# Optimization experiments

Hardware: AMD Instinct MI355X
Metric: run time of the kernel (lower is better)

## Reference

```python
import jax, jax.numpy as jnp
import numpy as np

B, S, D = 32, 512, 768
H = 12
HD = D // H
SCALE = HD ** -0.5


def setup_inputs() -> dict:
    key = jax.random.key(0)
    ks = jax.random.split(key, 5)
    return {
        "x": jax.random.normal(ks[0], (B, S, D), dtype=jnp.float32),
        "qkv_w": jax.random.normal(ks[1], (3 * D, D), dtype=jnp.float32) * (D ** -0.5),
        "qkv_b": jax.random.normal(ks[2], (3 * D,), dtype=jnp.float32) * 0.02,
        "proj_w": jax.random.normal(ks[3], (D, D), dtype=jnp.float32) * (D ** -0.5),
        "proj_b": jax.random.normal(ks[4], (D,), dtype=jnp.float32) * 0.02,
    }


def reference(x, qkv_w, qkv_b, proj_w, proj_b) -> jnp.ndarray:
    b, s, d = x.shape
    # fused QKV projection (torch Linear: x @ W.T + b)
    qkv = x @ qkv_w.T + qkv_b                      # [B,S,3D]
    qkv = qkv.reshape(b, s, 3, H, HD)
    qkv = jnp.transpose(qkv, (2, 0, 3, 1, 4))      # [3,B,H,S,HD]
    q, k, v = qkv[0], qkv[1], qkv[2]
    scores = jnp.einsum("bhqd,bhkd->bhqk", q, k) * SCALE  # [B,H,S,S]
    # attn_drop with p=0.0 (eval) -> identity
    attn = jax.nn.softmax(scores, axis=-1)
    out = jnp.einsum("bhqk,bhkd->bhqd", attn, v)   # [B,H,S,HD]
    out = jnp.transpose(out, (0, 2, 1, 3)).reshape(b, s, d)
    out = out @ proj_w.T + proj_b                  # proj_drop p=0.0 -> identity
    return out
```

## Files before the change

### kernel.cpp

```cpp
#include <hip/hip_runtime.h>
#include <hip/hip_bf16.h>

#define B_  32
#define S_  512
#define D_  768
#define H_  12
#define HD_ 64
#define QKV_ELEMS (B_ * H_ * S_ * HD_)

typedef __hip_bfloat16 bf16;
typedef short bf16x8_t __attribute__((ext_vector_type(8)));
typedef float f32x4_t  __attribute__((ext_vector_type(4)));

__device__ __forceinline__ float bf2f(bf16 x) { return __bfloat162float(x); }
__device__ __forceinline__ bf16  f2bf(float x) { return __float2bfloat16(x); }

__device__ __forceinline__ void gl_lds16(const short* g, short* l) {
    __builtin_amdgcn_global_load_lds(
        (const __attribute__((address_space(1))) void*)g,
        (__attribute__((address_space(3))) void*)l, 16, 0, 0);
}

__global__ __launch_bounds__(256) void f2bf_kernel(
    const float* __restrict__ in, unsigned short* __restrict__ out, int n4)
{
    int i = blockIdx.x * 256 + threadIdx.x;
    if (i >= n4) return;
    float4 v = reinterpret_cast<const float4*>(in)[i];
    ushort4 o;
    o.x = __bfloat16_as_ushort(f2bf(v.x));
    o.y = __bfloat16_as_ushort(f2bf(v.y));
    o.z = __bfloat16_as_ushort(f2bf(v.z));
    o.w = __bfloat16_as_ushort(f2bf(v.w));
    reinterpret_cast<ushort4*>(out)[i] = o;
}

#define GEMM_CORE(As, Bs, Aptr, Bptr, m0, n0, K)                               \
    const int t = threadIdx.x;                                                 \
    const int w = t >> 6, lane = t & 63;                                       \
    const int wr = w >> 1, wc = w & 1;                                         \
    const int quad = lane >> 4, l16 = lane & 15;                               \
    f32x4_t acc[4][4] = {};                                                    \
    const int lrow = lane >> 3;                                                \
    const int scol = (((lane & 7) ^ (lrow & 7)) * 8);                          \
    _Pragma("unroll")                                                          \
    for (int j = 0; j < 4; ++j) {                                              \
        int R = j * 32 + w * 8;                                                \
        gl_lds16((Aptr) + (size_t)((m0) + R + lrow) * (K) + scol, &(As)[R * 64]); \
        gl_lds16((Bptr) + (size_t)((n0) + R + lrow) * (K) + scol, &(Bs)[R * 64]); \
    }                                                                          \
    for (int k0 = 0; k0 < (K); k0 += 64) {                                     \
        const int curo = ((k0 >> 6) & 1) * 8192;                               \
        __syncthreads();                                                       \
        if (k0 + 64 < (K)) {                                                   \
            const int nxo = curo ^ 8192;                                       \
            _Pragma("unroll")                                                  \
            for (int j = 0; j < 4; ++j) {                                      \
                int R = j * 32 + w * 8;                                        \
                gl_lds16((Aptr) + (size_t)((m0) + R + lrow) * (K) + k0 + 64 + scol, \
                         &(As)[nxo + R * 64]);                                 \
                gl_lds16((Bptr) + (size_t)((n0) + R + lrow) * (K) + k0 + 64 + scol, \
                         &(Bs)[nxo + R * 64]);                                 \
            }                                                                  \
        }                                                                      \
        _Pragma("unroll")                                                      \
        for (int ks = 0; ks < 64; ks += 32) {                                  \
            bf16x8_t af[4], bf_[4];                                            \
            _Pragma("unroll")                                                  \
            for (int tm = 0; tm < 4; ++tm)                                     \
                af[tm] = *(const bf16x8_t*)&(As)[curo + (wr * 64 + tm * 16 + l16) * 64 \
                        + ((((ks >> 3) + quad) ^ (l16 & 7)) * 8)];             \
            _Pragma("unroll")                                                  \
            for (int tn = 0; tn < 4; ++tn)                                     \
                bf_[tn] = *(const bf16x8_t*)&(Bs)[curo + (wc * 64 + tn * 16 + l16) * 64 \
                        + ((((ks >> 3) + quad) ^ (l16 & 7)) * 8)];             \
            _Pragma("unroll")                                                  \
            for (int tm = 0; tm < 4; ++tm)                                     \
                _Pragma("unroll")                                              \
                for (int tn = 0; tn < 4; ++tn)                                 \
                    acc[tm][tn] = __builtin_amdgcn_mfma_f32_16x16x32_bf16(     \
                        af[tm], bf_[tn], acc[tm][tn], 0, 0, 0);                \
        }                                                                      \
    }

__global__ __launch_bounds__(256) void qkv_gemm_mfma(
    const short* __restrict__ A, const short* __restrict__ W,
    const float* __restrict__ bias,
    bf16* __restrict__ Q, bf16* __restrict__ Kp, bf16* __restrict__ Vp)
{
    __shared__ short As[2 * 128 * 64];
    __shared__ short Bs[2 * 128 * 64];
    const int n0 = blockIdx.x * 128;
    const int m0 = blockIdx.y * 128;
    GEMM_CORE(As, Bs, A, W, m0, n0, 768)

    const int which = n0 / 768;
    const int h = ((n0 + wc * 64) % 768) >> 6;
    bf16* dst = (which == 0) ? Q : (which == 1) ? Kp : Vp;
    float bv[4];
#pragma unroll
    for (int tn = 0; tn < 4; ++tn) bv[tn] = bias[n0 + wc * 64 + tn * 16 + l16];
#pragma unroll
    for (int tm = 0; tm < 4; ++tm) {
#pragma unroll
        for (int r = 0; r < 4; ++r) {
            int m = m0 + wr * 64 + tm * 16 + quad * 4 + r;
            int b = m >> 9, s = m & 511;
            size_t rb = (((size_t)b * H_ + h) * S_ + s) * HD_;
#pragma unroll
            for (int tn = 0; tn < 4; ++tn)
                dst[rb + tn * 16 + l16] = f2bf(acc[tm][tn][r] + bv[tn]);
        }
    }
}

__global__ __launch_bounds__(256) void proj_gemm_mfma(
    const short* __restrict__ A, const short* __restrict__ W,
    const float* __restrict__ bias, float* __restrict__ out)
{
    __shared__ short As[2 * 128 * 64];
    __shared__ short Bs[2 * 128 * 64];
    const int n0 = blockIdx.x * 128;
    const int m0 = blockIdx.y * 128;
    GEMM_CORE(As, Bs, A, W, m0, n0, 768)

    float bv[4];
#pragma unroll
    for (int tn = 0; tn < 4; ++tn) bv[tn] = bias[n0 + wc * 64 + tn * 16 + l16];
#pragma unroll
    for (int tm = 0; tm < 4; ++tm) {
#pragma unroll
        for (int r = 0; r < 4; ++r) {
            int m = m0 + wr * 64 + tm * 16 + quad * 4 + r;
#pragma unroll
            for (int tn = 0; tn < 4; ++tn)
                out[(size_t)m * 768 + n0 + wc * 64 + tn * 16 + l16] =
                    acc[tm][tn][r] + bv[tn];
        }
    }
}

#define QT 128
#define KT 64
#define PS 68
#define VS 68

__global__ __launch_bounds__(256, 3) void attn_mfma(
    const short* __restrict__ Qg, const short* __restrict__ Kg,
    const short* __restrict__ Vg, bf16* __restrict__ O)
{
    __shared__ short Qs[QT * 64];
    __shared__ short Ks[KT * 64];
    __shared__ short Vt[64 * VS];
    __shared__ short Ps[QT * PS];

    const int t = threadIdx.x;
    const int w = t >> 6, lane = t & 63;
    const int quad = lane >> 4, l16 = lane & 15;
    const int lrow = lane >> 3;
    const int scol = (((lane & 7) ^ (lrow & 7)) * 8);
    const int qt = blockIdx.x & 3;
    const int bh = blockIdx.x >> 2;
    const int q0 = qt * QT;
    const size_t base = (size_t)bh * (S_ * HD_);

#pragma unroll
    for (int j = 0; j < 4; ++j) {
        int R = j * 32 + w * 8;
        gl_lds16(Qg + base + (size_t)(q0 + R + lrow) * 64 + scol, &Qs[R * 64]);
    }

    const int wq = w * 32;
    f32x4_t Oacc[2][4] = {};
    float lsum[2][4] = {};

    for (int kt = 0; kt < S_; kt += KT) {
        __syncthreads();
#pragma unroll
        for (int j = 0; j < 2; ++j) {
            int R = j * 32 + w * 8;
            gl_lds16(Kg + base + (size_t)(kt + R + lrow) * 64 + scol, &Ks[R * 64]);
        }
        {
            int k = lane, dg = w;
            const bf16x8_t* gv = (const bf16x8_t*)(Vg + base + (size_t)(kt + k) * 64 + dg * 16);
            bf16x8_t v0 = gv[0], v1 = gv[1];
#pragma unroll
            for (int i = 0; i < 8; ++i) {
                Vt[(dg * 16 + i) * VS + k]     = v0[i];
                Vt[(dg * 16 + 8 + i) * VS + k] = v1[i];
            }
        }
        __syncthreads();

        f32x4_t sc[2][4] = {};
#pragma unroll
        for (int ks = 0; ks < 64; ks += 32) {
            bf16x8_t aq[2], bk[4];
#pragma unroll
            for (int tm = 0; tm < 2; ++tm)
                aq[tm] = *(const bf16x8_t*)&Qs[(wq + tm * 16 + l16) * 64
                        + ((((ks >> 3) + quad) ^ (l16 & 7)) * 8)];
#pragma unroll
            for (int tn = 0; tn < 4; ++tn)
                bk[tn] = *(const bf16x8_t*)&Ks[(tn * 16 + l16) * 64
                        + ((((ks >> 3) + quad) ^ (l16 & 7)) * 8)];
#pragma unroll
            for (int tm = 0; tm < 2; ++tm)
#pragma unroll
                for (int tn = 0; tn < 4; ++tn)
                    sc[tm][tn] = __builtin_amdgcn_mfma_f32_16x16x32_bf16(
                        aq[tm], bk[tn], sc[tm][tn], 0, 0, 0);
        }

#pragma unroll
        for (int tm = 0; tm < 2; ++tm) {
#pragma unroll
            for (int r = 0; r < 4; ++r) {
                int row = wq + tm * 16 + quad * 4 + r;
                float rs = 0.f;
#pragma unroll
                for (int tn = 0; tn < 4; ++tn) {
                    float p = __expf(sc[tm][tn][r] * 0.125f);
                    rs += p;
                    Ps[row * PS + tn * 16 + l16] = (short)__bfloat16_as_ushort(f2bf(p));
                }
                lsum[tm][r] += rs;
            }
        }

#pragma unroll
        for (int ks = 0; ks < 64; ks += 32) {
            bf16x8_t ap[2], bv[4];
#pragma unroll
            for (int tm = 0; tm < 2; ++tm)
                ap[tm] = *(const bf16x8_t*)&Ps[(wq + tm * 16 + l16) * PS + ks + quad * 8];
#pragma unroll
            for (int tn = 0; tn < 4; ++tn)
                bv[tn] = *(const bf16x8_t*)&Vt[(tn * 16 + l16) * VS + ks + quad * 8];
#pragma unroll
            for (int tm = 0; tm < 2; ++tm)
#pragma unroll
                for (int tn = 0; tn < 4; ++tn)
                    Oacc[tm][tn] = __builtin_amdgcn_mfma_f32_16x16x32_bf16(
                        ap[tm], bv[tn], Oacc[tm][tn], 0, 0, 0);
        }
    }

    float linv[2][4];
#pragma unroll
    for (int tm = 0; tm < 2; ++tm)
#pragma unroll
        for (int r = 0; r < 4; ++r) {
            float v = lsum[tm][r];
            v += __shfl_xor(v, 1, 64);
            v += __shfl_xor(v, 2, 64);
            v += __shfl_xor(v, 4, 64);
            v += __shfl_xor(v, 8, 64);
            linv[tm][r] = 1.f / v;
        }
    const int b = bh / H_, h = bh % H_;
#pragma unroll
    for (int tm = 0; tm < 2; ++tm) {
#pragma unroll
        for (int r = 0; r < 4; ++r) {
            int row = q0 + wq + tm * 16 + quad * 4 + r;
            size_t ob = ((size_t)b * S_ + row) * D_ + h * HD_;
#pragma unroll
            for (int tn = 0; tn < 4; ++tn)
                O[ob + tn * 16 + l16] = f2bf(Oacc[tm][tn][r] * linv[tm][r]);
        }
    }
}

extern "C" void kernel_launch(void* const* d_in, const int* in_sizes, int n_in,
                              void* d_out, int out_size, void* d_ws, size_t ws_size,
                              hipStream_t stream) {
    const float* x      = (const float*)d_in[0];
    const float* qkv_w  = (const float*)d_in[1];
    const float* qkv_b  = (const float*)d_in[2];
    const float* proj_w = (const float*)d_in[3];
    const float* proj_b = (const float*)d_in[4];
    float* out = (float*)d_out;

    unsigned short* q     = (unsigned short*)d_ws;
    unsigned short* k     = q + QKV_ELEMS;
    unsigned short* v     = k + QKV_ELEMS;
    unsigned short* slot4 = v + QKV_ELEMS;
    unsigned short* wq    = slot4 + QKV_ELEMS;
    unsigned short* wp    = wq + 2304 * 768;

    f2bf_kernel<<<(16384 * 768 / 4 + 255) / 256, 256, 0, stream>>>(x, slot4, 16384 * 768 / 4);
    f2bf_kernel<<<(2304 * 768 / 4 + 255) / 256, 256, 0, stream>>>(qkv_w, wq, 2304 * 768 / 4);
    f2bf_kernel<<<(768 * 768 / 4 + 255) / 256, 256, 0, stream>>>(proj_w, wp, 768 * 768 / 4);

    qkv_gemm_mfma<<<dim3(18, 128), 256, 0, stream>>>(
        (const short*)slot4, (const short*)wq, qkv_b,
        (bf16*)q, (bf16*)k, (bf16*)v);

    attn_mfma<<<dim3(32 * 12 * 4), 256, 0, stream>>>(
        (const short*)q, (const short*)k, (const short*)v, (bf16*)slot4);

    proj_gemm_mfma<<<dim3(6, 128), 256, 0, stream>>>(
        (const short*)slot4, (const short*)wp, proj_b, out);
}
```

Baseline: 278.0 us.

## Merge bf16 conversion launches and shrink GEMM K-tile for higher occupancy

The three fp32-to-bf16 conversion kernels are merged into one launch, which indexes into three source/destination pairs, to save launch overhead. The shared GEMM core's K-step is halved from 64 to 32, with a new 4-way XOR swizzle, which halves LDS per block and adds a launch-bounds hint of 5 blocks per SIMD-group. The aim is more resident blocks to hide memory latency. The cost is twice as many barriers and K iterations, with less MFMA work between each sync.

```diff
diff --git a/kernel.cpp b/kernel.cpp
--- a/kernel.cpp
+++ b/kernel.cpp
@@ -21,18 +21,24 @@
         (__attribute__((address_space(3))) void*)l, 16, 0, 0);
 }
 
-__global__ __launch_bounds__(256) void f2bf_kernel(
-    const float* __restrict__ in, unsigned short* __restrict__ out, int n4)
+__global__ __launch_bounds__(256) void f2bf3_kernel(
+    const float* __restrict__ a, unsigned short* __restrict__ oa, int na4,
+    const float* __restrict__ b, unsigned short* __restrict__ ob, int nb4,
+    const float* __restrict__ c, unsigned short* __restrict__ oc, int nc4)
 {
     int i = blockIdx.x * 256 + threadIdx.x;
-    if (i >= n4) return;
-    float4 v = reinterpret_cast<const float4*>(in)[i];
+    const float* src; unsigned short* dst; int idx;
+    if (i < na4)            { src = a; dst = oa; idx = i; }
+    else if (i < na4 + nb4) { src = b; dst = ob; idx = i - na4; }
+    else if (i < na4 + nb4 + nc4) { src = c; dst = oc; idx = i - na4 - nb4; }
+    else return;
+    float4 v = reinterpret_cast<const float4*>(src)[idx];
     ushort4 o;
     o.x = __bfloat16_as_ushort(f2bf(v.x));
     o.y = __bfloat16_as_ushort(f2bf(v.y));
     o.z = __bfloat16_as_ushort(f2bf(v.z));
     o.w = __bfloat16_as_ushort(f2bf(v.w));
-    reinterpret_cast<ushort4*>(out)[i] = o;
+    reinterpret_cast<ushort4*>(dst)[idx] = o;
 }
 
 #define GEMM_CORE(As, Bs, Aptr, Bptr, m0, n0, K)                               \
@@ -41,55 +47,51 @@
     const int wr = w >> 1, wc = w & 1;                                         \
     const int quad = lane >> 4, l16 = lane & 15;                               \
     f32x4_t acc[4][4] = {};                                                    \
-    const int lrow = lane >> 3;                                                \
-    const int scol = (((lane & 7) ^ (lrow & 7)) * 8);                          \
+    const int lrow2 = lane >> 2;                                               \
+    const int scol2 = (((lane & 3) ^ (lrow2 & 3)) * 8);                        \
+    const int rsw = ((quad ^ (l16 & 3)) * 8);                                  \
     _Pragma("unroll")                                                          \
-    for (int j = 0; j < 4; ++j) {                                              \
-        int R = j * 32 + w * 8;                                                \
-        gl_lds16((Aptr) + (size_t)((m0) + R + lrow) * (K) + scol, &(As)[R * 64]); \
-        gl_lds16((Bptr) + (size_t)((n0) + R + lrow) * (K) + scol, &(Bs)[R * 64]); \
+    for (int j = 0; j < 2; ++j) {                                              \
+        int R = j * 64 + w * 16;                                               \
+        gl_lds16((Aptr) + (size_t)((m0) + R + lrow2) * (K) + scol2, &(As)[R * 32]); \
+        gl_lds16((Bptr) + (size_t)((n0) + R + lrow2) * (K) + scol2, &(Bs)[R * 32]); \
     }                                                                          \
-    for (int k0 = 0; k0 < (K); k0 += 64) {                                     \
-        const int curo = ((k0 >> 6) & 1) * 8192;                               \
+    for (int k0 = 0; k0 < (K); k0 += 32) {                                     \
+        const int curo = ((k0 >> 5) & 1) * 4096;                               \
         __syncthreads();                                                       \
-        if (k0 + 64 < (K)) {                                                   \
-            const int nxo = curo ^ 8192;                                       \
+        if (k0 + 32 < (K)) {                                                   \
+            const int nxo = curo ^ 4096;                                       \
             _Pragma("unroll")                                                  \
-            for (int j = 0; j < 4; ++j) {                                      \
-                int R = j * 32 + w * 8;                                        \
-                gl_lds16((Aptr) + (size_t)((m0) + R + lrow) * (K) + k0 + 64 + scol, \
-                         &(As)[nxo + R * 64]);                                 \
-                gl_lds16((Bptr) + (size_t)((n0) + R + lrow) * (K) + k0 + 64 + scol, \
-                         &(Bs)[nxo + R * 64]);                                 \
+            for (int j = 0; j < 2; ++j) {                                      \
+                int R = j * 64 + w * 16;                                       \
+                gl_lds16((Aptr) + (size_t)((m0) + R + lrow2) * (K) + k0 + 32 + scol2, \
+                         &(As)[nxo + R * 32]);                                 \
+                gl_lds16((Bptr) + (size_t)((n0) + R + lrow2) * (K) + k0 + 32 + scol2, \
+                         &(Bs)[nxo + R * 32]);                                 \
             }                                                                  \
         }                                                                      \
+        bf16x8_t af[4], bf_[4];                                                \
         _Pragma("unroll")                                                      \
-        for (int ks = 0; ks < 64; ks += 32) {                                  \
-            bf16x8_t af[4], bf_[4];                                            \
-            _Pragma("unroll")                                                  \
-            for (int tm = 0; tm < 4; ++tm)                                     \
-                af[tm] = *(const bf16x8_t*)&(As)[curo + (wr * 64 + tm * 16 + l16) * 64 \
-                        + ((((ks >> 3) + quad) ^ (l16 & 7)) * 8)];             \
+        for (int tm = 0; tm < 4; ++tm)                                         \
+            af[tm] = *(const bf16x8_t*)&(As)[curo + (wr * 64 + tm * 16 + l16) * 32 + rsw]; \
+        _Pragma("unroll")                                                      \
+        for (int tn = 0; tn < 4; ++tn)                                         \
+            bf_[tn] = *(const bf16x8_t*)&(Bs)[curo + (wc * 64 + tn * 16 + l16) * 32 + rsw]; \
+        _Pragma("unroll")                                                      \
+        for (int tm = 0; tm < 4; ++tm)                                         \
             _Pragma("unroll")                                                  \
             for (int tn = 0; tn < 4; ++tn)                                     \
-                bf_[tn] = *(const bf16x8_t*)&(Bs)[curo + (wc * 64 + tn * 16 + l16) * 64 \
-                        + ((((ks >> 3) + quad) ^ (l16 & 7)) * 8)];             \
-            _Pragma("unroll")                                                  \
-            for (int tm = 0; tm < 4; ++tm)                                     \
-                _Pragma("unroll")                                              \
-                for (int tn = 0; tn < 4; ++tn)                                 \
-                    acc[tm][tn] = __builtin_amdgcn_mfma_f32_16x16x32_bf16(     \
-                        af[tm], bf_[tn], acc[tm][tn], 0, 0, 0);                \
-        }                                                                      \
-    }
-
-__global__ __launch_bounds__(256) void qkv_gemm_mfma(
+                acc[tm][tn] = __builtin_amdgcn_mfma_f32_16x16x32_bf16(         \
+                    af[tm], bf_[tn], acc[tm][tn], 0, 0, 0);                    \
+    }
+
+__global__ __launch_bounds__(256, 5) void qkv_gemm_mfma(
     const short* __restrict__ A, const short* __restrict__ W,
     const float* __restrict__ bias,
     bf16* __restrict__ Q, bf16* __restrict__ Kp, bf16* __restrict__ Vp)
 {
-    __shared__ short As[2 * 128 * 64];
-    __shared__ short Bs[2 * 128 * 64];
+    __shared__ short As[2 * 128 * 32];
+    __shared__ short Bs[2 * 128 * 32];
     const int n0 = blockIdx.x * 128;
     const int m0 = blockIdx.y * 128;
     GEMM_CORE(As, Bs, A, W, m0, n0, 768)
@@ -114,12 +116,12 @@
     }
 }
 
-__global__ __launch_bounds__(256) void proj_gemm_mfma(
+__global__ __launch_bounds__(256, 5) void proj_gemm_mfma(
     const short* __restrict__ A, const short* __restrict__ W,
     const float* __restrict__ bias, float* __restrict__ out)
 {
-    __shared__ short As[2 * 128 * 64];
-    __shared__ short Bs[2 * 128 * 64];
+    __shared__ short As[2 * 128 * 32];
+    __shared__ short Bs[2 * 128 * 32];
     const int n0 = blockIdx.x * 128;
     const int m0 = blockIdx.y * 128;
     GEMM_CORE(As, Bs, A, W, m0, n0, 768)
@@ -290,9 +292,9 @@
     unsigned short* wq    = slot4 + QKV_ELEMS;
     unsigned short* wp    = wq + 2304 * 768;
 
-    f2bf_kernel<<<(16384 * 768 / 4 + 255) / 256, 256, 0, stream>>>(x, slot4, 16384 * 768 / 4);
-    f2bf_kernel<<<(2304 * 768 / 4 + 255) / 256, 256, 0, stream>>>(qkv_w, wq, 2304 * 768 / 4);
-    f2bf_kernel<<<(768 * 768 / 4 + 255) / 256, 256, 0, stream>>>(proj_w, wp, 768 * 768 / 4);
+    const int nx4 = 16384 * 768 / 4, nq4 = 2304 * 768 / 4, np4 = 768 * 768 / 4;
+    f2bf3_kernel<<<(nx4 + nq4 + np4 + 255) / 256, 256, 0, stream>>>(
+        x, slot4, nx4, qkv_w, wq, nq4, proj_w, wp, np4);
 
     qkv_gemm_mfma<<<dim3(18, 128), 256, 0, stream>>>(
         (const short*)slot4, (const short*)wq, qkv_b,
```

Measured after the change: 562.3 us. +102.2%, slower.
